# Kernel tuning notes

Hardware: AMD Instinct MI355X
Metric: run time of the kernel (lower is better)

The kernel has to match this reference:

```python
import jax, jax.numpy as jnp
import numpy as np

B, S, TEXT_DIM, VISION_DIM, HIDDEN, HEADS = 4, 2048, 768, 768, 512, 8
HEAD_DIM = HIDDEN // HEADS


def setup_inputs() -> dict:
    key = jax.random.key(0)
    ks = jax.random.split(key, 9)
    s_in = 1.0 / np.sqrt(TEXT_DIM)
    s_h = 1.0 / np.sqrt(HIDDEN)
    return {
        "text_embeds": jax.random.normal(ks[0], (B, S, TEXT_DIM), dtype=jnp.float32),
        "Wq": jax.random.uniform(ks[1], (TEXT_DIM, HIDDEN), jnp.float32, -s_in, s_in),
        "bq": jax.random.uniform(ks[2], (HIDDEN,), jnp.float32, -s_in, s_in),
        "Wk": jax.random.uniform(ks[3], (TEXT_DIM, HIDDEN), jnp.float32, -s_in, s_in),
        "bk": jax.random.uniform(ks[4], (HIDDEN,), jnp.float32, -s_in, s_in),
        "Wv": jax.random.uniform(ks[5], (TEXT_DIM, HIDDEN), jnp.float32, -s_in, s_in),
        "bv": jax.random.uniform(ks[6], (HIDDEN,), jnp.float32, -s_in, s_in),
        "Wo": jax.random.uniform(ks[7], (HIDDEN, VISION_DIM), jnp.float32, -s_h, s_h),
        "bo": jax.random.uniform(ks[8], (VISION_DIM,), jnp.float32, -s_h, s_h),
    }


def reference(text_embeds, Wq, bq, Wk, bk, Wv, bv, Wo, bo):
    b, s, _ = text_embeds.shape
    # QKV projections -> [b, heads, s, head_dim]
    def proj(W, bias):
        y = jnp.einsum("bsd,dh->bsh", text_embeds, W) + bias
        return y.reshape(b, s, HEADS, HEAD_DIM).transpose(0, 2, 1, 3)
    q, k, v = proj(Wq, bq), proj(Wk, bk), proj(Wv, bv)
    scores = jnp.einsum("bhqd,bhkd->bhqk", q, k) / np.sqrt(HEAD_DIM).astype(np.float32)
    weights = jax.nn.softmax(scores, axis=-1)
    attended = jnp.einsum("bhqk,bhkd->bhqd", weights, v)
    attended = attended.transpose(0, 2, 1, 3).reshape(b, s, HIDDEN)
    out = jnp.einsum("bsh,hv->bsv", attended, Wo) + bo
    return jnp.squeeze(out, axis=1) if out.shape[1] == 1 else out
```

## Files before the change

### kernel.cpp

```cpp
#include <hip/hip_runtime.h>
#include <hip/hip_bf16.h>

#define BATCH 4
#define SEQ 2048
#define TDIM 768
#define VDIM 768
#define HID 512
#define NHEADS 8
#define HDIM 64
#define MROWS (BATCH * SEQ)
#define NQKV (3 * HID)

typedef unsigned short ushort_t;
typedef __attribute__((ext_vector_type(8))) short short8;
typedef __attribute__((ext_vector_type(4))) short short4v;
typedef __attribute__((ext_vector_type(4))) float floatx4;

#define QSCALE 0.18033688011112042f

__device__ __forceinline__ ushort_t bf16_rne(float f) {
    unsigned int u = __float_as_uint(f);
    u = (u + 0x7fffu + ((u >> 16) & 1u)) >> 16;
    return (ushort_t)u;
}

__device__ __forceinline__ void async16(const ushort_t* g, ushort_t* l) {
    __builtin_amdgcn_global_load_lds(
        (const __attribute__((address_space(1))) unsigned int*)g,
        (__attribute__((address_space(3))) unsigned int*)l, 16, 0, 0);
}

__global__ __launch_bounds__(256) void conv_x(const float* __restrict__ X,
                                              ushort_t* __restrict__ Xb)
{
    const int i = (blockIdx.x * 256 + threadIdx.x) * 4;
    const floatx4 v = *(const floatx4*)(X + i);
    short4v o;
#pragma unroll
    for (int j = 0; j < 4; ++j) o[j] = (short)bf16_rne(v[j]);
    *(short4v*)(Xb + i) = o;
}

__global__ __launch_bounds__(256) void transp_w(
    const float* __restrict__ Wq, const float* __restrict__ Wk,
    const float* __restrict__ Wv, const float* __restrict__ Wo,
    ushort_t* __restrict__ Wqkvt, ushort_t* __restrict__ Wot)
{
    __shared__ float tile[32][33];
    const int z = blockIdx.z;
    const float* src;
    ushort_t* dst;
    int R, C;
    if (z < 3) {
        src = (z == 0) ? Wq : (z == 1) ? Wk : Wv;
        dst = Wqkvt + (size_t)z * HID * TDIM;
        R = TDIM; C = HID;
    } else {
        src = Wo; dst = Wot; R = HID; C = VDIM;
    }
    const int tx = threadIdx.x & 31, ty = threadIdx.x >> 5;
    const int c0 = blockIdx.x * 32, r0 = blockIdx.y * 32;
    if (c0 >= C || r0 >= R) return;
#pragma unroll
    for (int i = 0; i < 4; ++i)
        tile[ty + i * 8][tx] = src[(size_t)(r0 + ty + i * 8) * C + c0 + tx];
    __syncthreads();
#pragma unroll
    for (int i = 0; i < 4; ++i)
        dst[(size_t)(c0 + ty + i * 8) * R + r0 + tx] = bf16_rne(tile[tx][ty + i * 8]);
}

template<int KD, bool SWAPPED>
__device__ __forceinline__ void gemm128(
    const ushort_t* __restrict__ A, const ushort_t* __restrict__ Bt,
    int m0, int n0, ushort_t* As, ushort_t* Bs, floatx4 (&acc)[4][4])
{
    const int tid  = threadIdx.x;
    const int lane = tid & 63;
    const int w    = tid >> 6;
    const int l15  = lane & 15;
    const int quad = lane >> 4;
    const int wrow = w >> 1;
    const int wcol = w & 1;

    const int srow = lane >> 3;
    const int scol = (lane & 7) * 8;

    const ushort_t* ga = A  + (size_t)(m0 + w * 32 + srow) * KD + scol;
    const ushort_t* gb = Bt + (size_t)(n0 + w * 32 + srow) * KD + scol;
    ushort_t* la = As + (w * 32) * 64;
    ushort_t* lb = Bs + (w * 32) * 64;

    for (int kt = 0; kt < KD; kt += 64) {
#pragma unroll
        for (int i = 0; i < 4; ++i) {
            async16(ga + (size_t)(i * 8) * KD + kt, la + i * 8 * 64);
            async16(gb + (size_t)(i * 8) * KD + kt, lb + i * 8 * 64);
        }
        __syncthreads();
#pragma unroll
        for (int half = 0; half < 2; ++half) {
            const int kk = half * 32 + quad * 8;
            short8 af[4], bf[4];
#pragma unroll
            for (int t = 0; t < 4; ++t) {
                af[t] = *(const short8*)&As[(wrow * 64 + t * 16 + l15) * 64 + kk];
                bf[t] = *(const short8*)&Bs[(wcol * 64 + t * 16 + l15) * 64 + kk];
            }
#pragma unroll
            for (int mi = 0; mi < 4; ++mi)
#pragma unroll
                for (int ni = 0; ni < 4; ++ni) {
                    if (SWAPPED)
                        acc[mi][ni] = __builtin_amdgcn_mfma_f32_16x16x32_bf16(
                            bf[ni], af[mi], acc[mi][ni], 0, 0, 0);
                    else
                        acc[mi][ni] = __builtin_amdgcn_mfma_f32_16x16x32_bf16(
                            af[mi], bf[ni], acc[mi][ni], 0, 0, 0);
                }
        }
        __syncthreads();
    }
}

__global__ __launch_bounds__(256) void qkv_gemm_mfma(
    const ushort_t* __restrict__ Xb, const ushort_t* __restrict__ Wt,
    const float* __restrict__ bq, const float* __restrict__ bk,
    const float* __restrict__ bv,
    ushort_t* __restrict__ Q, ushort_t* __restrict__ K, ushort_t* __restrict__ V)
{
    __shared__ __align__(16) ushort_t As[128 * 64];
    __shared__ __align__(16) ushort_t Bs[128 * 64];

    const int bx = blockIdx.x;
    const int m0 = blockIdx.y * 128;
    const int n0 = bx * 128;
    const int which = bx >> 2;
    const bool isV = (which == 2);

    floatx4 acc[4][4];
#pragma unroll
    for (int i = 0; i < 4; ++i)
#pragma unroll
        for (int j = 0; j < 4; ++j) acc[i][j] = (floatx4)0.0f;

    if (isV) gemm128<TDIM, false>(Xb, Wt, m0, n0, As, Bs, acc);
    else     gemm128<TDIM, true >(Xb, Wt, m0, n0, As, Bs, acc);

    const int lane = threadIdx.x & 63;
    const int w    = threadIdx.x >> 6;
    const int l15  = lane & 15;
    const int quad = lane >> 4;
    const int wrow = w >> 1;
    const int wcol = w & 1;

    if (!isV) {
        const float* bias = (which == 0) ? bq : bk;
        const float scale = (which == 0) ? QSCALE : 1.0f;
        ushort_t* Out = (which == 0) ? Q : K;
#pragma unroll
        for (int mi = 0; mi < 4; ++mi) {
            const int m = m0 + wrow * 64 + mi * 16 + l15;
            const int b = m >> 11;
            const int s = m & 2047;
#pragma unroll
            for (int ni = 0; ni < 4; ++ni) {
                const int c = (n0 - which * HID) + wcol * 64 + ni * 16 + quad * 4;
                const int h = c >> 6;
                const int d0 = c & 63;
                const floatx4 b4 = *(const floatx4*)(bias + c);
                short4v pk;
#pragma unroll
                for (int r = 0; r < 4; ++r)
                    pk[r] = (short)bf16_rne((acc[mi][ni][r] + b4[r]) * scale);
                *(short4v*)&Out[((size_t)(b * NHEADS + h) * SEQ + s) * HDIM + d0] = pk;
            }
        }
    } else {
#pragma unroll
        for (int ni = 0; ni < 4; ++ni) {
            const int c = (n0 - 2 * HID) + wcol * 64 + ni * 16 + l15;
            const int h = c >> 6;
            const int d = c & 63;
            const float b1 = bv[c];
#pragma unroll
            for (int mi = 0; mi < 4; ++mi) {
                const int mb = m0 + wrow * 64 + mi * 16 + quad * 4;
                const int b = mb >> 11;
                const int s0 = mb & 2047;
                short4v pk;
#pragma unroll
                for (int r = 0; r < 4; ++r)
                    pk[r] = (short)bf16_rne(acc[mi][ni][r] + b1);
                *(short4v*)&V[((size_t)(b * NHEADS + h) * HDIM + d) * SEQ + s0] = pk;
            }
        }
    }
}

#define KSTR 72
#define PSTR 72

__global__ __launch_bounds__(512) void flash_attn_mfma(
    const ushort_t* __restrict__ Q, const ushort_t* __restrict__ K,
    const ushort_t* __restrict__ Vt, ushort_t* __restrict__ Att)
{
    __shared__ __align__(16) ushort_t Ks[2][64 * KSTR];
    __shared__ __align__(16) ushort_t Vs[2][64 * KSTR];
    __shared__ __align__(16) ushort_t Ps[8][16 * PSTR];

    const int tid  = threadIdx.x;
    const int lane = tid & 63;
    const int w    = tid >> 6;
    const int l15  = lane & 15;
    const int quad = lane >> 4;

    const int bh = blockIdx.y;
    const int b  = bh >> 3;
    const int h  = bh & 7;
    const int q0 = blockIdx.x * 128;

    const ushort_t* Qb = Q  + (size_t)bh * SEQ * HDIM;
    const ushort_t* Kb = K  + (size_t)bh * SEQ * HDIM;
    const ushort_t* Vb = Vt + (size_t)bh * HDIM * SEQ;

    short8 qf0, qf1;
    {
        const ushort_t* qrow = Qb + (size_t)(q0 + w * 16 + l15) * HDIM + quad * 8;
        qf0 = *(const short8*)(qrow);
        qf1 = *(const short8*)(qrow + 32);
    }

    float l_run = 0.f;
    floatx4 of[4];
#pragma unroll
    for (int t = 0; t < 4; ++t) of[t] = (floatx4)0.0f;

    const int srow = tid >> 3;
    const int sseg = (tid & 7) * 8;

    const ushort_t* gk = Kb + (size_t)srow * HDIM + sseg;
    const ushort_t* gv = Vb + (size_t)srow * SEQ + sseg;
    const int lofs = srow * KSTR + sseg;

    short8 kreg = *(const short8*)(gk);
    short8 vreg = *(const short8*)(gv);

    int buf = 0;
    for (int kt = 0; kt < SEQ; kt += 64) {
        *(short8*)&Ks[buf][lofs] = kreg;
        *(short8*)&Vs[buf][lofs] = vreg;
        __syncthreads();

        if (kt + 64 < SEQ) {
            kreg = *(const short8*)(gk + (size_t)(kt + 64) * HDIM);
            vreg = *(const short8*)(gv + (kt + 64));
        }

        floatx4 sacc[4];
#pragma unroll
        for (int t = 0; t < 4; ++t) {
            const short8 kf0 = *(const short8*)&Ks[buf][(t * 16 + l15) * KSTR + quad * 8];
            const short8 kf1 = *(const short8*)&Ks[buf][(t * 16 + l15) * KSTR + 32 + quad * 8];
            floatx4 a = (floatx4)0.0f;
            a = __builtin_amdgcn_mfma_f32_16x16x32_bf16(kf0, qf0, a, 0, 0, 0);
            a = __builtin_amdgcn_mfma_f32_16x16x32_bf16(kf1, qf1, a, 0, 0, 0);
            sacc[t] = a;
        }

        float p[4][4];
        float rs = 0.f;
#pragma unroll
        for (int t = 0; t < 4; ++t)
#pragma unroll
            for (int r = 0; r < 4; ++r) {
                const float e = exp2f(sacc[t][r]);
                p[t][r] = e;
                rs += e;
            }
        l_run += rs;

#pragma unroll
        for (int t = 0; t < 4; ++t) {
            const unsigned u0 = __float_as_uint(p[t][0]) + 0x8000u;
            const unsigned u1 = __float_as_uint(p[t][1]) + 0x8000u;
            const unsigned u2 = __float_as_uint(p[t][2]) + 0x8000u;
            const unsigned u3 = __float_as_uint(p[t][3]) + 0x8000u;
            unsigned pk2[2];
            pk2[0] = __builtin_amdgcn_perm(u1, u0, 0x07060302u);
            pk2[1] = __builtin_amdgcn_perm(u3, u2, 0x07060302u);
            *(unsigned long long*)&Ps[w][l15 * PSTR + t * 16 + quad * 4] =
                ((unsigned long long)pk2[1] << 32) | pk2[0];
        }
        asm volatile("s_waitcnt lgkmcnt(0)" ::: "memory");

        const short8 pf0 = *(const short8*)&Ps[w][l15 * PSTR + quad * 8];
        const short8 pf1 = *(const short8*)&Ps[w][l15 * PSTR + 32 + quad * 8];

#pragma unroll
        for (int t = 0; t < 4; ++t) {
            const short8 vf0 = *(const short8*)&Vs[buf][(t * 16 + l15) * KSTR + quad * 8];
            const short8 vf1 = *(const short8*)&Vs[buf][(t * 16 + l15) * KSTR + 32 + quad * 8];
            of[t] = __builtin_amdgcn_mfma_f32_16x16x32_bf16(vf0, pf0, of[t], 0, 0, 0);
            of[t] = __builtin_amdgcn_mfma_f32_16x16x32_bf16(vf1, pf1, of[t], 0, 0, 0);
        }
        buf ^= 1;
    }

    l_run += __shfl_xor(l_run, 16);
    l_run += __shfl_xor(l_run, 32);
    const float inv = 1.f / l_run;

    const int s = q0 + w * 16 + l15;
    ushort_t* arow = Att + ((size_t)(b * SEQ + s)) * HID + h * HDIM;
#pragma unroll
    for (int t = 0; t < 4; ++t) {
        short4v pk;
#pragma unroll
        for (int r = 0; r < 4; ++r) pk[r] = (short)bf16_rne(of[t][r] * inv);
        *(short4v*)&arow[t * 16 + quad * 4] = pk;
    }
}

__global__ __launch_bounds__(256) void out_gemm_mfma(
    const ushort_t* __restrict__ Attb, const ushort_t* __restrict__ Wot,
    const float* __restrict__ bo, float* __restrict__ Y)
{
    __shared__ __align__(16) ushort_t As[128 * 64];
    __shared__ __align__(16) ushort_t Bs[128 * 64];

    const int m0 = blockIdx.y * 128;
    const int n0 = blockIdx.x * 128;

    floatx4 acc[4][4];
#pragma unroll
    for (int i = 0; i < 4; ++i)
#pragma unroll
        for (int j = 0; j < 4; ++j) acc[i][j] = (floatx4)0.0f;

    gemm128<HID, true>(Attb, Wot, m0, n0, As, Bs, acc);

    const int lane = threadIdx.x & 63;
    const int w    = threadIdx.x >> 6;
    const int l15  = lane & 15;
    const int quad = lane >> 4;
    const int wrow = w >> 1;
    const int wcol = w & 1;

#pragma unroll
    for (int mi = 0; mi < 4; ++mi) {
        const int m = m0 + wrow * 64 + mi * 16 + l15;
#pragma unroll
        for (int ni = 0; ni < 4; ++ni) {
            const int nb = n0 + wcol * 64 + ni * 16 + quad * 4;
            const floatx4 b4 = *(const floatx4*)(bo + nb);
            floatx4 o;
#pragma unroll
            for (int r = 0; r < 4; ++r) o[r] = acc[mi][ni][r] + b4[r];
            *(floatx4*)&Y[(size_t)m * VDIM + nb] = o;
        }
    }
}

extern "C" void kernel_launch(void* const* d_in, const int* in_sizes, int n_in,
                              void* d_out, int out_size, void* d_ws, size_t ws_size,
                              hipStream_t stream)
{
    const float* text = (const float*)d_in[0];
    const float* Wq = (const float*)d_in[1];
    const float* bq = (const float*)d_in[2];
    const float* Wk = (const float*)d_in[3];
    const float* bk = (const float*)d_in[4];
    const float* Wv = (const float*)d_in[5];
    const float* bv = (const float*)d_in[6];
    const float* Wo = (const float*)d_in[7];
    const float* bo = (const float*)d_in[8];
    float* out = (float*)d_out;

    ushort_t* Xb    = (ushort_t*)d_ws;
    ushort_t* Wqkvt = Xb + (size_t)MROWS * TDIM;
    ushort_t* Wot   = Wqkvt + (size_t)NQKV * TDIM;
    ushort_t* Qw    = Wot + (size_t)VDIM * HID;
    ushort_t* Kw    = Qw + (size_t)MROWS * HID;
    ushort_t* Vtw   = Kw + (size_t)MROWS * HID;
    ushort_t* Attb  = Vtw + (size_t)MROWS * HID;

    conv_x<<<dim3(MROWS * TDIM / 1024), 256, 0, stream>>>(text, Xb);
    transp_w<<<dim3(24, 24, 4), 256, 0, stream>>>(Wq, Wk, Wv, Wo, Wqkvt, Wot);
    qkv_gemm_mfma<<<dim3(12, 64), 256, 0, stream>>>(Xb, Wqkvt, bq, bk, bv, Qw, Kw, Vtw);
    flash_attn_mfma<<<dim3(16, 32), 512, 0, stream>>>(Qw, Kw, Vtw, Attb);
    out_gemm_mfma<<<dim3(6, 64), 256, 0, stream>>>(Attb, Wot, bo, out);
}
```

Before: 215.9 us.

## Restructure flash attention loop with async LDS loads and register P transpose

```diff
diff --git a/kernel.cpp b/kernel.cpp
--- a/kernel.cpp
+++ b/kernel.cpp
@@ -198,16 +198,12 @@
     }
 }
 
-#define KSTR 72
-#define PSTR 72
-
 __global__ __launch_bounds__(512) void flash_attn_mfma(
     const ushort_t* __restrict__ Q, const ushort_t* __restrict__ K,
     const ushort_t* __restrict__ Vt, ushort_t* __restrict__ Att)
 {
-    __shared__ __align__(16) ushort_t Ks[2][64 * KSTR];
-    __shared__ __align__(16) ushort_t Vs[2][64 * KSTR];
-    __shared__ __align__(16) ushort_t Ps[8][16 * PSTR];
+    __shared__ __align__(16) ushort_t Ks[2][64 * 64];
+    __shared__ __align__(16) ushort_t Vs[2][64 * 64];
 
     const int tid  = threadIdx.x;
     const int lane = tid & 63;
@@ -231,85 +227,104 @@
         qf1 = *(const short8*)(qrow + 32);
     }
 
-    float l_run = 0.f;
     floatx4 of[4];
 #pragma unroll
     for (int t = 0; t < 4; ++t) of[t] = (floatx4)0.0f;
-
-    const int srow = tid >> 3;
-    const int sseg = (tid & 7) * 8;
-
-    const ushort_t* gk = Kb + (size_t)srow * HDIM + sseg;
-    const ushort_t* gv = Vb + (size_t)srow * SEQ + sseg;
-    const int lofs = srow * KSTR + sseg;
-
-    short8 kreg = *(const short8*)(gk);
-    short8 vreg = *(const short8*)(gv);
-
-    int buf = 0;
-    for (int kt = 0; kt < SEQ; kt += 64) {
-        *(short8*)&Ks[buf][lofs] = kreg;
-        *(short8*)&Vs[buf][lofs] = vreg;
-        __syncthreads();
-
-        if (kt + 64 < SEQ) {
-            kreg = *(const short8*)(gk + (size_t)(kt + 64) * HDIM);
-            vreg = *(const short8*)(gv + (kt + 64));
-        }
-
+    floatx4 ofl = (floatx4)0.0f;
+
+    short8 ones;
+#pragma unroll
+    for (int j = 0; j < 8; ++j) ones[j] = (short)0x3F80;
+
+    const floatx4 z4 = (floatx4)0.0f;
+
+    const int srow = lane >> 3;
+    const int scol = ((lane & 7) ^ srow) * 8;
+    const ushort_t* gk = Kb + (size_t)(w * 8 + srow) * HDIM + scol;
+    const ushort_t* gv = Vb + (size_t)(w * 8 + srow) * SEQ + scol;
+    ushort_t* lk0 = &Ks[0][w * 8 * 64];
+    ushort_t* lk1 = &Ks[1][w * 8 * 64];
+    ushort_t* lv0 = &Vs[0][w * 8 * 64];
+    ushort_t* lv1 = &Vs[1][w * 8 * 64];
+
+    const int off0 = (quad ^ (l15 & 7)) * 8;
+    const int off1 = off0 ^ 32;
+
+    auto tile = [&](const ushort_t* Kt, const ushort_t* Vt_) {
         floatx4 sacc[4];
+        __builtin_amdgcn_s_setprio(1);
 #pragma unroll
         for (int t = 0; t < 4; ++t) {
-            const short8 kf0 = *(const short8*)&Ks[buf][(t * 16 + l15) * KSTR + quad * 8];
-            const short8 kf1 = *(const short8*)&Ks[buf][(t * 16 + l15) * KSTR + 32 + quad * 8];
-            floatx4 a = (floatx4)0.0f;
+            const short8 kf0 = *(const short8*)&Kt[(t * 16 + l15) * 64 + off0];
+            const short8 kf1 = *(const short8*)&Kt[(t * 16 + l15) * 64 + off1];
+            floatx4 a = z4;
             a = __builtin_amdgcn_mfma_f32_16x16x32_bf16(kf0, qf0, a, 0, 0, 0);
             a = __builtin_amdgcn_mfma_f32_16x16x32_bf16(kf1, qf1, a, 0, 0, 0);
             sacc[t] = a;
         }
-
-        float p[4][4];
-        float rs = 0.f;
-#pragma unroll
-        for (int t = 0; t < 4; ++t)
-#pragma unroll
-            for (int r = 0; r < 4; ++r) {
-                const float e = exp2f(sacc[t][r]);
-                p[t][r] = e;
-                rs += e;
-            }
-        l_run += rs;
-
+        __builtin_amdgcn_s_setprio(0);
+
+        unsigned w0[4], w1[4];
 #pragma unroll
         for (int t = 0; t < 4; ++t) {
-            const unsigned u0 = __float_as_uint(p[t][0]) + 0x8000u;
-            const unsigned u1 = __float_as_uint(p[t][1]) + 0x8000u;
-            const unsigned u2 = __float_as_uint(p[t][2]) + 0x8000u;
-            const unsigned u3 = __float_as_uint(p[t][3]) + 0x8000u;
-            unsigned pk2[2];
-            pk2[0] = __builtin_amdgcn_perm(u1, u0, 0x07060302u);
-            pk2[1] = __builtin_amdgcn_perm(u3, u2, 0x07060302u);
-            *(unsigned long long*)&Ps[w][l15 * PSTR + t * 16 + quad * 4] =
-                ((unsigned long long)pk2[1] << 32) | pk2[0];
-        }
-        asm volatile("s_waitcnt lgkmcnt(0)" ::: "memory");
-
-        const short8 pf0 = *(const short8*)&Ps[w][l15 * PSTR + quad * 8];
-        const short8 pf1 = *(const short8*)&Ps[w][l15 * PSTR + 32 + quad * 8];
-
+            const float p0 = __builtin_amdgcn_exp2f(sacc[t][0]);
+            const float p1 = __builtin_amdgcn_exp2f(sacc[t][1]);
+            const float p2 = __builtin_amdgcn_exp2f(sacc[t][2]);
+            const float p3 = __builtin_amdgcn_exp2f(sacc[t][3]);
+            asm("v_cvt_pk_bf16_f32 %0, %1, %2" : "=v"(w0[t]) : "v"(p0), "v"(p1));
+            asm("v_cvt_pk_bf16_f32 %0, %1, %2" : "=v"(w1[t]) : "v"(p2), "v"(p3));
+        }
+
+        unsigned a0 = w0[0], b0 = w0[1];
+        asm("v_permlane32_swap_b32 %0, %1" : "+v"(a0), "+v"(b0));
+        asm("v_permlane16_swap_b32 %0, %1" : "+v"(a0), "+v"(b0));
+        unsigned a1 = w1[0], b1 = w1[1];
+        asm("v_permlane32_swap_b32 %0, %1" : "+v"(a1), "+v"(b1));
+        asm("v_permlane16_swap_b32 %0, %1" : "+v"(a1), "+v"(b1));
+        unsigned a2 = w0[2], b2 = w0[3];
+        asm("v_permlane32_swap_b32 %0, %1" : "+v"(a2), "+v"(b2));
+        asm("v_permlane16_swap_b32 %0, %1" : "+v"(a2), "+v"(b2));
+        unsigned a3 = w1[2], b3 = w1[3];
+        asm("v_permlane32_swap_b32 %0, %1" : "+v"(a3), "+v"(b3));
+        asm("v_permlane16_swap_b32 %0, %1" : "+v"(a3), "+v"(b3));
+
+        union { unsigned u[4]; short8 s; } P0, P1;
+        P0.u[0] = a0; P0.u[1] = a1; P0.u[2] = b0; P0.u[3] = b1;
+        P1.u[0] = a2; P1.u[1] = a3; P1.u[2] = b2; P1.u[3] = b3;
+        const short8 pf0 = P0.s;
+        const short8 pf1 = P1.s;
+
+        __builtin_amdgcn_s_setprio(1);
+        ofl = __builtin_amdgcn_mfma_f32_16x16x32_bf16(ones, pf0, ofl, 0, 0, 0);
+        ofl = __builtin_amdgcn_mfma_f32_16x16x32_bf16(ones, pf1, ofl, 0, 0, 0);
 #pragma unroll
         for (int t = 0; t < 4; ++t) {
-            const short8 vf0 = *(const short8*)&Vs[buf][(t * 16 + l15) * KSTR + quad * 8];
-            const short8 vf1 = *(const short8*)&Vs[buf][(t * 16 + l15) * KSTR + 32 + quad * 8];
+            const short8 vf0 = *(const short8*)&Vt_[(t * 16 + l15) * 64 + off0];
+            const short8 vf1 = *(const short8*)&Vt_[(t * 16 + l15) * 64 + off1];
             of[t] = __builtin_amdgcn_mfma_f32_16x16x32_bf16(vf0, pf0, of[t], 0, 0, 0);
             of[t] = __builtin_amdgcn_mfma_f32_16x16x32_bf16(vf1, pf1, of[t], 0, 0, 0);
         }
-        buf ^= 1;
-    }
-
-    l_run += __shfl_xor(l_run, 16);
-    l_run += __shfl_xor(l_run, 32);
-    const float inv = 1.f / l_run;
+        __builtin_amdgcn_s_setprio(0);
+    };
+
+    async16(gk, lk0);
+    async16(gv, lv0);
+
+    for (int kt = 0; kt < SEQ; kt += 128) {
+        __syncthreads();
+        async16(gk + (size_t)(kt + 64) * HDIM, lk1);
+        async16(gv + (kt + 64), lv1);
+        tile(Ks[0], Vs[0]);
+
+        __syncthreads();
+        if (kt + 128 < SEQ) {
+            async16(gk + (size_t)(kt + 128) * HDIM, lk0);
+            async16(gv + (kt + 128), lv0);
+        }
+        tile(Ks[1], Vs[1]);
+    }
+
+    const float inv = 1.f / ofl[0];
 
     const int s = q0 + w * 16 + l15;
     ushort_t* arow = Att + ((size_t)(b * SEQ + s)) * HID + h * HDIM;
```

Measured after the change: 197.0 us. 8.8% less time.
